# Kernel tuning notes

Measured on AMD Instinct MI355X. Metric: run time of the kernel, lower is better.

Reference implementation:

```python
import jax, jax.numpy as jnp
import numpy as np

B, S, D, H = 128, 256, 256, 8   # graphs, nodes/graph, dim_h, heads
N = B * S
E = 524288
DH = D // H
BN_EPS = 1e-5

def _bn(v, g, b):
    # BatchNorm1d forward with batch statistics (biased var), eval-dropout model
    m = v.mean(0)
    var = v.var(0)
    return (v - m) * jax.lax.rsqrt(var + BN_EPS) * g + b

def setup_inputs() -> dict:
    key = jax.random.key(0)
    ks = jax.random.split(key, 40)
    x = jax.random.normal(ks[0], (N, D), jnp.float32)
    src = jax.random.randint(ks[1], (E,), 0, N)
    dst = (src // S) * S + jax.random.randint(ks[2], (E,), 0, S)  # intra-graph edges
    edge_index = jnp.stack([src, dst]).astype(jnp.int64)
    def lin(k, i, o):
        return (jax.random.normal(k, (i, o), jnp.float32) / np.float32(np.sqrt(i)))
    inp = {
        'x': x, 'edge_index': edge_index,
        'W_gcn': lin(ks[3], D, D), 'b_gcn': jnp.zeros((D,), jnp.float32),
        'W_gin1': lin(ks[4], D, D), 'b_gin1': jnp.zeros((D,), jnp.float32),
        'W_gin2': lin(ks[5], D, D), 'b_gin2': jnp.zeros((D,), jnp.float32),
        'g_kv': jnp.ones((D,), jnp.float32), 'be_kv': jnp.zeros((D,), jnp.float32),
        'Wq1': lin(ks[6], D, D), 'bq1': jnp.zeros((D,), jnp.float32),
        'Wq2': lin(ks[7], D, D), 'bq2': jnp.zeros((D,), jnp.float32),
        'Wq_a': lin(ks[8], D, D), 'bq_a': jnp.zeros((D,), jnp.float32),
        'Wk_a': lin(ks[9], D, D), 'bk_a': jnp.zeros((D,), jnp.float32),
        'Wv_a': lin(ks[10], D, D), 'bv_a': jnp.zeros((D,), jnp.float32),
        'Wo_a': lin(ks[11], D, D), 'bo_a': jnp.zeros((D,), jnp.float32),
        'g_attn': jnp.ones((D,), jnp.float32), 'be_attn': jnp.zeros((D,), jnp.float32),
        'Wf1': lin(ks[12], D, 2 * D), 'bf1': jnp.zeros((2 * D,), jnp.float32),
        'Wf2': lin(ks[13], 2 * D, D), 'bf2': jnp.zeros((D,), jnp.float32),
        'g2': jnp.ones((D,), jnp.float32), 'be2': jnp.zeros((D,), jnp.float32),
    }
    return inp

def _forward(x, edge_index,
             W_gcn, b_gcn, W_gin1, b_gin1, W_gin2, b_gin2, g_kv, be_kv,
             Wq1, bq1, Wq2, bq2,
             Wq_a, bq_a, Wk_a, bk_a, Wv_a, bv_a, Wo_a, bo_a, g_attn, be_attn,
             Wf1, bf1, Wf2, bf2, g2, be2):
    row, col = edge_index[0], edge_index[1]
    h_in1 = x

    # ---- expert 0: GCNConv (add self loops + symmetric norm) ----
    loops = jnp.arange(N, dtype=row.dtype)
    row2 = jnp.concatenate([row, loops])
    col2 = jnp.concatenate([col, loops])
    deg = jax.ops.segment_sum(jnp.ones_like(row2, jnp.float32), col2, num_segments=N)
    dinv = jnp.where(deg > 0, jax.lax.rsqrt(deg), 0.0)
    norm = dinv[row2] * dinv[col2]                     # [E+N]
    xw = x @ W_gcn                                      # [N, D]
    h_gcn = jax.ops.segment_sum(norm[:, None] * xw[row2], col2, num_segments=N) + b_gcn
    e0 = _bn(h_gcn, g_kv, be_kv)

    # ---- expert 1: GINConv (eps=0, sum aggregation, 2-layer MLP) ----
    agg = jax.ops.segment_sum(x[row], col, num_segments=N)
    h_gin = jax.nn.relu((x + agg) @ W_gin1 + b_gin1) @ W_gin2 + b_gin2
    e1 = _bn(h_gin, g_kv, be_kv)

    # ---- global expert normalization (torch .std -> unbiased) ----
    allo = jnp.concatenate([e0, e1], axis=0)
    gm = allo.mean()
    gs = jnp.std(allo, ddof=1)
    e0 = (e0 - gm) / (gs + 1e-8)
    e1 = (e1 - gm) / (gs + 1e-8)

    # ---- uniform routing & kv residual mix ----
    kv = 0.5 * e0 + 0.5 * e1 + 0.1 * h_in1              # [N, D]

    # ---- dense batching (equal-sized graphs -> pure reshape, full mask) ----
    q_dense = h_in1.reshape(B, S, D)
    kv_dense = kv.reshape(B, S, D)

    # ---- q projection MLP ----
    q_dense = jax.nn.relu(q_dense @ Wq1 + bq1) @ Wq2 + bq2

    # ---- multihead attention (batch_first, no padding) ----
    qh = (q_dense @ Wq_a + bq_a).reshape(B, S, H, DH)
    kh = (kv_dense @ Wk_a + bk_a).reshape(B, S, H, DH)
    vh = (kv_dense @ Wv_a + bv_a).reshape(B, S, H, DH)
    scores = jnp.einsum('bqhd,bkhd->bhqk', qh, kh) / np.float32(np.sqrt(DH))
    attn = jax.nn.softmax(scores, axis=-1)
    o = jnp.einsum('bhqk,bkhd->bqhd', attn, vh).reshape(B, S, D)
    h_attn = (o @ Wo_a + bo_a).reshape(N, D)

    # ---- residual + norm + FFN block ----
    h = _bn(h_in1 + h_attn, g_attn, be_attn)
    h_ff = jax.nn.relu(h @ Wf1 + bf1) @ Wf2 + bf2
    h = _bn(h + h_ff, g2, be2)
    return h

def reference(x, edge_index,
              W_gcn, b_gcn, W_gin1, b_gin1, W_gin2, b_gin2, g_kv, be_kv,
              Wq1, bq1, Wq2, bq2,
              Wq_a, bq_a, Wk_a, bk_a, Wv_a, bv_a, Wo_a, bo_a, g_attn, be_attn,
              Wf1, bf1, Wf2, bf2, g2, be2):
    return _forward(x, edge_index,
                    W_gcn, b_gcn, W_gin1, b_gin1, W_gin2, b_gin2, g_kv, be_kv,
                    Wq1, bq1, Wq2, bq2,
                    Wq_a, bq_a, Wk_a, bk_a, Wv_a, bv_a, Wo_a, bo_a, g_attn, be_attn,
                    Wf1, bf1, Wf2, bf2, g2, be2)
```

## Files before the change

kernel.cpp:

```cpp
#include <hip/hip_runtime.h>
#include <hip/hip_bf16.h>

typedef __hip_bfloat16 bf16;
typedef __attribute__((ext_vector_type(8))) short short8;
typedef __attribute__((ext_vector_type(4))) short short4v;
typedef __attribute__((ext_vector_type(4))) float f32x4;

#define N_ 32768
#define D_ 256
#define S_ 256
#define B_ 128
#define E_ 524288

static __device__ __forceinline__ f32x4 mfma16(short8 a, short8 b, f32x4 c) {
  return __builtin_amdgcn_mfma_f32_16x16x32_bf16(a, b, c, 0, 0, 0);
}
static __device__ __forceinline__ f32x4 fzero4() {
  f32x4 z; z[0] = 0.f; z[1] = 0.f; z[2] = 0.f; z[3] = 0.f; return z;
}
static __device__ __forceinline__ float bits2f(short s) {
  unsigned u = ((unsigned)(unsigned short)s) << 16;
  return __builtin_bit_cast(float, u);
}
static __device__ __forceinline__ short f2bits(float f) {
  bf16 b = __float2bfloat16(f);
  return __builtin_bit_cast(short, b);
}
static __device__ __forceinline__ float tof(float x) { return x; }
static __device__ __forceinline__ float tof(bf16 x) { return __bfloat162float(x); }

#define GLOAD_LDS16(G, L) __builtin_amdgcn_global_load_lds( \
    (const __attribute__((address_space(1))) void*)(G),     \
    (__attribute__((address_space(3))) void*)(L), 16, 0, 0)

template<int F>
__global__ __launch_bounds__(256)
void gemm_bt(const bf16* __restrict__ A, const bf16* __restrict__ Bt,
             const float* __restrict__ bias, const void* __restrict__ resid,
             float* __restrict__ Cf, bf16* __restrict__ Cb,
             float* __restrict__ Sp, float* __restrict__ SSp,
             int M, int Nc, int K, long bsA, long bsB, long bsC)
{
  __shared__ __align__(16) bf16 lA[128 * 32];
  __shared__ __align__(16) bf16 lB[128 * 32];
  __shared__ float sS[2][128], sSS[2][128];
  const int z = blockIdx.z;
  const bf16* Ab = A + (long)z * bsA;
  const bf16* Bb = Bt + (long)z * bsB;
  const int m0 = blockIdx.x * 128, n0 = blockIdx.y * 128;
  const int tid = threadIdx.x;
  const int lane = tid & 63;
  const int w = tid >> 6, wr = w >> 1, wc = w & 1;
  const int g = lane >> 4, r = lane & 15, ko = g * 8;
  const int srow = lane >> 2, skw = (lane & 3) * 8;

  f32x4 acc[4][4];
  for (int i = 0; i < 4; i++) for (int j = 0; j < 4; j++) acc[i][j] = fzero4();

  for (int k0 = 0; k0 < K; k0 += 32) {
    __syncthreads();
    for (int i = 0; i < 2; i++) {
      const int c = w * 2 + i;
      GLOAD_LDS16(Ab + (long)(m0 + c * 16 + srow) * K + k0 + skw, lA + c * 512);
      GLOAD_LDS16(Bb + (long)(n0 + c * 16 + srow) * K + k0 + skw, lB + c * 512);
    }
    __syncthreads();
    short8 af[4], bfv[4];
    for (int mi = 0; mi < 4; mi++)
      af[mi] = *(const short8*)&lA[(wr * 64 + mi * 16 + r) * 32 + ko];
    for (int ni = 0; ni < 4; ni++)
      bfv[ni] = *(const short8*)&lB[(wc * 64 + ni * 16 + r) * 32 + ko];
    for (int mi = 0; mi < 4; mi++)
      for (int ni = 0; ni < 4; ni++)
        acc[mi][ni] = mfma16(af[mi], bfv[ni], acc[mi][ni]);
  }

  float cs[4] = {0, 0, 0, 0}, css[4] = {0, 0, 0, 0};
  for (int mi = 0; mi < 4; mi++) for (int ni = 0; ni < 4; ni++) {
    const int row = m0 + wr * 64 + mi * 16 + g * 4;
    const int col = n0 + wc * 64 + ni * 16 + r;
    float bv = (F & 2) ? bias[col] : 0.0f;
    for (int j = 0; j < 4; j++) {
      long idx = (long)(row + j) * Nc + col;
      float v = acc[mi][ni][j] + bv;
      if (F & 4)  v += ((const float*)resid)[(long)z * bsC + idx];
      if (F & 64) v += bits2f(((const short*)resid)[(long)z * bsC + idx]);
      if (F & 1)  v = fmaxf(v, 0.0f);
      if (F & 32) { cs[ni] += v; css[ni] += v * v; }
      if (F & 8)  Cf[(long)z * bsC + idx] = v;
      if (F & 16) Cb[(long)z * bsC + idx] = __float2bfloat16(v);
    }
  }
  if (F & 32) {
    for (int ni = 0; ni < 4; ni++) {
      cs[ni]  += __shfl_xor(cs[ni], 16);  cs[ni]  += __shfl_xor(cs[ni], 32);
      css[ni] += __shfl_xor(css[ni], 16); css[ni] += __shfl_xor(css[ni], 32);
    }
    if (lane < 16) {
      for (int ni = 0; ni < 4; ni++) {
        sS[wr][wc * 64 + ni * 16 + lane]  = cs[ni];
        sSS[wr][wc * 64 + ni * 16 + lane] = css[ni];
      }
    }
    __syncthreads();
    if (tid < 128) {
      atomicAdd(&Sp[n0 + tid],  sS[0][tid] + sS[1][tid]);
      atomicAdd(&SSp[n0 + tid], sSS[0][tid] + sSS[1][tid]);
    }
  }
}

__global__ __launch_bounds__(256)
void attn_k(const bf16* __restrict__ qh, const bf16* __restrict__ kh,
            const bf16* __restrict__ vh, bf16* __restrict__ ob)
{
  const int qt = blockIdx.x, h = blockIdx.y, b = blockIdx.z;
  const int tid = threadIdx.x, lane = tid & 63, w = tid >> 6;
  const int g = lane >> 4, r = lane & 15, ko = g * 8;
  __shared__ __align__(16) bf16 lQ[64 * 40];
  __shared__ __align__(16) bf16 lK[256 * 40];
  __shared__ __align__(16) bf16 lV[32 * 264];
  __shared__ __align__(16) bf16 lP[4][16 * 264];

  { int row = tid >> 2, c = (tid & 3) * 8;
    *(short8*)&lQ[row * 40 + c] =
      *(const short8*)(qh + (long)(b * 256 + qt * 64 + row) * 256 + h * 32 + c); }
  for (int i = 0; i < 4; i++) {
    int s = tid + i * 256; int row = s >> 2, c = (s & 3) * 8;
    *(short8*)&lK[row * 40 + c] =
      *(const short8*)(kh + (long)(b * 256 + row) * 256 + h * 32 + c);
  }
  const bf16* vbp = vh + (long)b * 65536 + h * 32;
  for (int i = 0; i < 4; i++) {
    int q = tid + i * 256;
    int s = q >> 2, part = q & 3;
    short8 v = *(const short8*)(vbp + (long)s * 256 + part * 8);
    for (int j = 0; j < 8; j++)
      ((short*)lV)[(part * 8 + j) * 264 + s] = v[j];
  }
  __syncthreads();

  short8 aq = *(const short8*)&lQ[(w * 16 + r) * 40 + ko];
  f32x4 sc[16];
  for (int nc = 0; nc < 16; nc++) {
    short8 bk = *(const short8*)&lK[(nc * 16 + r) * 40 + ko];
    sc[nc] = mfma16(aq, bk, fzero4());
  }
  const float scale = 0.17677669529663687f;
  float rsum[4];
  for (int j = 0; j < 4; j++) {
    float mx = -3.4e38f;
    for (int nc = 0; nc < 16; nc++) mx = fmaxf(mx, sc[nc][j]);
    mx = fmaxf(mx, __shfl_xor(mx, 1));
    mx = fmaxf(mx, __shfl_xor(mx, 2));
    mx = fmaxf(mx, __shfl_xor(mx, 4));
    mx = fmaxf(mx, __shfl_xor(mx, 8));
    float sum = 0.f;
    for (int nc = 0; nc < 16; nc++) {
      float p = __expf((sc[nc][j] - mx) * scale);
      sc[nc][j] = p; sum += p;
    }
    sum += __shfl_xor(sum, 1); sum += __shfl_xor(sum, 2);
    sum += __shfl_xor(sum, 4); sum += __shfl_xor(sum, 8);
    rsum[j] = sum;
    for (int nc = 0; nc < 16; nc++)
      lP[w][(g * 4 + j) * 264 + nc * 16 + r] = __float2bfloat16(sc[nc][j]);
  }
  __syncthreads();
  f32x4 oa[2]; oa[0] = fzero4(); oa[1] = fzero4();
  for (int kc = 0; kc < 8; kc++) {
    short8 ap = *(const short8*)&lP[w][r * 264 + kc * 32 + ko];
    for (int n = 0; n < 2; n++) {
      short8 bv = *(const short8*)&lV[(n * 16 + r) * 264 + kc * 32 + ko];
      oa[n] = mfma16(ap, bv, oa[n]);
    }
  }
  for (int n = 0; n < 2; n++) for (int j = 0; j < 4; j++) {
    float v = oa[n][j] / rsum[j];
    ob[(long)(b * 256 + qt * 64 + w * 16 + g * 4 + j) * 256 + h * 32 + n * 16 + r] =
      __float2bfloat16(v);
  }
}

template<typename TIN>
__global__ __launch_bounds__(256)
void transpose_cast_k(const TIN* __restrict__ in, bf16* __restrict__ out,
                      int in_rs, int out_rs, long zhi, long out_zs)
{
  __shared__ float tile[32][33];
  const int z = blockIdx.z;
  const long ioff = (long)z * zhi;
  const long ooff = (long)z * out_zs;
  const int tx = threadIdx.x, ty = threadIdx.y;
  const int c = blockIdx.x * 32 + tx;
  const int rb = blockIdx.y * 32;
  for (int i = 0; i < 4; i++)
    tile[ty + i * 8][tx] = tof(in[ioff + (long)(rb + ty + i * 8) * in_rs + c]);
  __syncthreads();
  const int oc = rb + tx;
  const int orb = blockIdx.x * 32;
  for (int i = 0; i < 4; i++)
    out[ooff + (long)(orb + ty + i * 8) * out_rs + oc] =
      __float2bfloat16(tile[tx][ty + i * 8]);
}

__global__ __launch_bounds__(256)
void w9t_k(const float* w0, const float* w1, const float* w2, const float* w3,
           const float* w4, const float* w5, const float* w6, const float* w7,
           const float* w8, bf16* __restrict__ out)
{
  __shared__ float tile[32][33];
  const float* srcs[9] = {w0, w1, w2, w3, w4, w5, w6, w7, w8};
  const int wi = blockIdx.z;
  const float* in = srcs[wi];
  bf16* o = out + (long)wi * 65536;
  const int tx = threadIdx.x, ty = threadIdx.y;
  const int c = blockIdx.x * 32 + tx;
  const int rb = blockIdx.y * 32;
  for (int i = 0; i < 4; i++)
    tile[ty + i * 8][tx] = in[(rb + ty + i * 8) * 256 + c];
  __syncthreads();
  const int oc = rb + tx;
  const int orb = blockIdx.x * 32;
  for (int i = 0; i < 4; i++)
    o[(orb + ty + i * 8) * 256 + oc] = __float2bfloat16(tile[tx][ty + i * 8]);
}

__global__ __launch_bounds__(256)
void cast4_k(const float* __restrict__ in, bf16* __restrict__ out)
{
  long i = ((long)blockIdx.x * 256 + threadIdx.x) * 4;
  float4 v = *(const float4*)(in + i);
  short4v o;
  o[0] = f2bits(v.x); o[1] = f2bits(v.y); o[2] = f2bits(v.z); o[3] = f2bits(v.w);
  *(short4v*)(out + i) = o;
}

__global__ __launch_bounds__(256)
void edge_cnt_k(const int* __restrict__ ei, float* __restrict__ cnt)
{
  int e = blockIdx.x * 256 + threadIdx.x;
  int src = ei[e], dst = ei[E_ + e];
  long idx = ((long)(src >> 8) * 256 + (dst & 255)) * 256 + (src & 255);
  atomicAdd(&cnt[idx], 1.0f);
}

__global__ __launch_bounds__(256)
void deg_k(const float* __restrict__ cnt, float* __restrict__ dinv)
{
  int rid = blockIdx.x * 16 + (threadIdx.x >> 4);
  int l16 = threadIdx.x & 15;
  const float4* rp = (const float4*)(cnt + (long)rid * 256);
  float s = 0.f;
  for (int i = 0; i < 4; i++) {
    float4 v = rp[l16 + i * 16];
    s += v.x + v.y + v.z + v.w;
  }
  s += __shfl_xor(s, 1); s += __shfl_xor(s, 2);
  s += __shfl_xor(s, 4); s += __shfl_xor(s, 8);
  if (l16 == 0) dinv[rid] = rsqrtf(s + 1.0f);
}

__global__ __launch_bounds__(256)
void adj_derive_k(const float* __restrict__ cnt, const float* __restrict__ dinv,
                  bf16* __restrict__ gin, bf16* __restrict__ gcn)
{
  long i = ((long)blockIdx.x * 256 + threadIdx.x) * 4;
  float4 c = *(const float4*)(cnt + i);
  long row = i >> 8;
  int g = (int)(row >> 8), dst = (int)(row & 255);
  int src0 = (int)(i & 255);
  float dd = dinv[row];
  const float* ds = dinv + (long)g * 256 + src0;
  float cv[4] = {c.x, c.y, c.z, c.w};
  short4v oi, oc;
  for (int j = 0; j < 4; j++) {
    float gv = cv[j] * dd * ds[j];
    if (src0 + j == dst) gv += dd * dd;
    oi[j] = f2bits(cv[j]);
    oc[j] = f2bits(gv);
  }
  *(short4v*)(gin + i) = oi;
  *(short4v*)(gcn + i) = oc;
}

__global__ __launch_bounds__(256)
void expert_stats_k(const float* __restrict__ S0, const float* __restrict__ SS0,
                    const float* __restrict__ S1, const float* __restrict__ SS1,
                    const float* __restrict__ gkv, const float* __restrict__ bkv,
                    float* __restrict__ kA, float* __restrict__ kB,
                    float* __restrict__ kC)
{
  const int d = threadIdx.x;
  const float invN = 1.0f / 32768.0f;
  float m0 = S0[d] * invN, v0 = SS0[d] * invN - m0 * m0;
  float a0 = gkv[d] * rsqrtf(v0 + 1e-5f), c0 = bkv[d] - m0 * a0;
  float m1 = S1[d] * invN, v1 = SS1[d] * invN - m1 * m1;
  float a1 = gkv[d] * rsqrtf(v1 + 1e-5f), c1 = bkv[d] - m1 * a1;
  float gsum = a0 * S0[d] + 32768.0f * c0 + a1 * S1[d] + 32768.0f * c1;
  float gss  = a0 * a0 * SS0[d] + 2.0f * a0 * c0 * S0[d] + 32768.0f * c0 * c0
             + a1 * a1 * SS1[d] + 2.0f * a1 * c1 * S1[d] + 32768.0f * c1 * c1;
  __shared__ float r1[256], r2[256];
  r1[d] = gsum; r2[d] = gss;
  __syncthreads();
  for (int s = 128; s > 0; s >>= 1) {
    if (d < s) { r1[d] += r1[d + s]; r2[d] += r2[d + s]; }
    __syncthreads();
  }
  const float cntall = 16777216.0f;
  float tg = r1[0], tss = r2[0];
  float gm = tg / cntall;
  float var = (tss - tg * tg / cntall) / (cntall - 1.0f);
  float gs = sqrtf(fmaxf(var, 0.f)) + 1e-8f;
  kA[d] = 0.5f * a0 / gs;
  kB[d] = 0.5f * a1 / gs;
  kC[d] = 0.5f * (c0 + c1 - 2.0f * gm) / gs;
}

__global__ __launch_bounds__(256)
void kv_mix_k(const bf16* __restrict__ hgcn, const bf16* __restrict__ hgin,
              const bf16* __restrict__ xb, const float* __restrict__ kA,
              const float* __restrict__ kB, const float* __restrict__ kC,
              bf16* __restrict__ kv)
{
  long i = ((long)blockIdx.x * 256 + threadIdx.x) * 8;
  int d0 = (int)(i & 255);
  short8 a = *(const short8*)(hgcn + i);
  short8 b = *(const short8*)(hgin + i);
  short8 c = *(const short8*)(xb + i);
  short8 o;
  for (int j = 0; j < 8; j++) {
    int d = d0 + j;
    float v = kA[d] * bits2f(a[j]) + kB[d] * bits2f(b[j]) + kC[d] + 0.1f * bits2f(c[j]);
    o[j] = f2bits(v);
  }
  *(short8*)(kv + i) = o;
}

template<int MODE>
__global__ __launch_bounds__(256)
void bn_apply_k(const bf16* __restrict__ in, const float* __restrict__ S,
                const float* __restrict__ SSq, const float* __restrict__ gg,
                const float* __restrict__ bb, float* __restrict__ outf,
                bf16* __restrict__ outb)
{
  long i = ((long)blockIdx.x * 256 + threadIdx.x) * 8;
  int d0 = (int)(i & 255);
  short8 v = *(const short8*)(in + i);
  const float invN = 1.0f / 32768.0f;
  float4 o0, o1; short8 o8;
  for (int j = 0; j < 8; j++) {
    int d = d0 + j;
    float m = S[d] * invN;
    float var = SSq[d] * invN - m * m;
    float a = gg[d] * rsqrtf(var + 1e-5f);
    float c = bb[d] - m * a;
    float o = a * bits2f(v[j]) + c;
    if (MODE & 1) { if (j < 4) (&o0.x)[j] = o; else (&o1.x)[j - 4] = o; }
    if (MODE & 2) o8[j] = f2bits(o);
  }
  if (MODE & 1) { *(float4*)(outf + i) = o0; *(float4*)(outf + i + 4) = o1; }
  if (MODE & 2) *(short8*)(outb + i) = o8;
}

static constexpr size_t OFF_S0 = 0, OFF_SS0 = 1024, OFF_S1 = 2048, OFF_SS1 = 3072;
static constexpr size_t OFF_S2 = 4096, OFF_SS2 = 5120, OFF_S3 = 6144, OFF_SS3 = 7168;
static constexpr size_t OFF_KA = 8192, OFF_KB = 9216, OFF_KC = 10240;
static constexpr size_t OFF_CNT = 16384;
static constexpr size_t ADJ_BYTES = (size_t)B_ * S_ * S_ * 4;
static constexpr size_t ZERO_BYTES = OFF_CNT + ADJ_BYTES;
static constexpr size_t OFF_DINV = ZERO_BYTES;
static constexpr size_t OFF_W = OFF_DINV + 131072;
static constexpr size_t NDB2 = (size_t)N_ * D_ * 2;
static constexpr size_t OFF_ADJGINB = OFF_W + 1703936;
static constexpr size_t OFF_ADJGCNB = OFF_ADJGINB + NDB2;
static constexpr size_t OFF_XB   = OFF_ADJGCNB + NDB2;
static constexpr size_t OFF_XT   = OFF_XB + NDB2;
static constexpr size_t OFF_XWB  = OFF_XT + NDB2;
static constexpr size_t OFF_XWT  = OFF_XWB + NDB2;
static constexpr size_t OFF_KV   = OFF_XWT + NDB2;
static constexpr size_t OFF_HGCN = OFF_KV + NDB2;
static constexpr size_t OFF_HGIN = OFF_HGCN + NDB2;

extern "C" void kernel_launch(void* const* d_in, const int* in_sizes, int n_in,
                              void* d_out, int out_size, void* d_ws, size_t ws_size,
                              hipStream_t stream)
{
  (void)in_sizes; (void)n_in; (void)out_size; (void)ws_size;
  const float* x      = (const float*)d_in[0];
  const int*   ei     = (const int*)d_in[1];
  const float* W_gcn  = (const float*)d_in[2];
  const float* b_gcn  = (const float*)d_in[3];
  const float* W_gin1 = (const float*)d_in[4];
  const float* b_gin1 = (const float*)d_in[5];
  const float* W_gin2 = (const float*)d_in[6];
  const float* b_gin2 = (const float*)d_in[7];
  const float* g_kv   = (const float*)d_in[8];
  const float* be_kv  = (const float*)d_in[9];
  const float* Wq1    = (const float*)d_in[10];
  const float* bq1    = (const float*)d_in[11];
  const float* Wq2    = (const float*)d_in[12];
  const float* bq2    = (const float*)d_in[13];
  const float* Wq_a   = (const float*)d_in[14];
  const float* bq_a   = (const float*)d_in[15];
  const float* Wk_a   = (const float*)d_in[16];
  const float* bk_a   = (const float*)d_in[17];
  const float* Wv_a   = (const float*)d_in[18];
  const float* bv_a   = (const float*)d_in[19];
  const float* Wo_a   = (const float*)d_in[20];
  const float* bo_a   = (const float*)d_in[21];
  const float* g_attn = (const float*)d_in[22];
  const float* be_attn= (const float*)d_in[23];
  const float* Wf1    = (const float*)d_in[24];
  const float* bf1    = (const float*)d_in[25];
  const float* Wf2    = (const float*)d_in[26];
  const float* bf2    = (const float*)d_in[27];
  const float* g2     = (const float*)d_in[28];
  const float* be2    = (const float*)d_in[29];

  char* ws = (char*)d_ws;
  float* S0  = (float*)(ws + OFF_S0);  float* SS0 = (float*)(ws + OFF_SS0);
  float* S1  = (float*)(ws + OFF_S1);  float* SS1 = (float*)(ws + OFF_SS1);
  float* S2  = (float*)(ws + OFF_S2);  float* SS2 = (float*)(ws + OFF_SS2);
  float* S3  = (float*)(ws + OFF_S3);  float* SS3 = (float*)(ws + OFF_SS3);
  float* kA  = (float*)(ws + OFF_KA);  float* kB  = (float*)(ws + OFF_KB);
  float* kC  = (float*)(ws + OFF_KC);
  float* cntA = (float*)(ws + OFF_CNT);
  float* dinv = (float*)(ws + OFF_DINV);
  bf16* wT = (bf16*)(ws + OFF_W);
  bf16 *WgcnT = wT,            *Wgin1T = wT + 65536,  *Wgin2T = wT + 131072;
  bf16 *Wq1T  = wT + 196608,   *Wq2T   = wT + 262144, *WqaT   = wT + 327680;
  bf16 *WkaT  = wT + 393216,   *WvaT   = wT + 458752, *WoaT   = wT + 524288;
  bf16 *Wf1T  = wT + 589824,   *Wf2T   = wT + 720896;
  bf16* adjGINb = (bf16*)(ws + OFF_ADJGINB);
  bf16* adjGCNb = (bf16*)(ws + OFF_ADJGCNB);
  bf16* xb    = (bf16*)(ws + OFF_XB);
  bf16* xT    = (bf16*)(ws + OFF_XT);
  bf16* xw_bf = (bf16*)(ws + OFF_XWB);
  bf16* xwT   = (bf16*)(ws + OFF_XWT);
  bf16* kv_bf = (bf16*)(ws + OFF_KV);
  bf16* hgcnb = (bf16*)(ws + OFF_HGCN);
  bf16* hginb = (bf16*)(ws + OFF_HGIN);
  bf16* gin_in = xw_bf;
  bf16* gin_h  = adjGCNb;
  bf16* qhb    = adjGCNb;
  bf16* khb    = adjGINb;
  bf16* q1b    = xT;
  bf16* qb     = xw_bf;
  bf16* vhb    = hgcnb;
  bf16* ob     = hginb;
  bf16* tbufb  = (bf16*)(ws + OFF_CNT);
  bf16* hb     = xb;
  bf16* f1b    = (bf16*)(ws + OFF_XWT);
  bf16* t2b    = adjGCNb;
  float* outp  = (float*)d_out;

  hipMemsetAsync(d_ws, 0, ZERO_BYTES, stream);

  dim3 tb(32, 8);
  w9t_k<<<dim3(8, 8, 9), tb, 0, stream>>>(W_gcn, W_gin1, W_gin2, Wq1, Wq2,
                                          Wq_a, Wk_a, Wv_a, Wo_a, wT);
  transpose_cast_k<float><<<dim3(16, 8, 1), tb, 0, stream>>>(Wf1, Wf1T, 512, 256, 0, 0);
  transpose_cast_k<float><<<dim3(8, 16, 1), tb, 0, stream>>>(Wf2, Wf2T, 256, 512, 0, 0);
  cast4_k<<<8192, 256, 0, stream>>>(x, xb);
  transpose_cast_k<float><<<dim3(8, 8, 128), tb, 0, stream>>>(x, xT, 256, 256, 65536, 65536);
  edge_cnt_k<<<2048, 256, 0, stream>>>(ei, cntA);
  deg_k<<<2048, 256, 0, stream>>>(cntA, dinv);
  adj_derive_k<<<8192, 256, 0, stream>>>(cntA, dinv, adjGINb, adjGCNb);
  gemm_bt<16><<<dim3(256, 2, 1), 256, 0, stream>>>(xb, WgcnT, nullptr, nullptr,
      nullptr, xw_bf, nullptr, nullptr, N_, 256, 256, 0, 0, 0);
  transpose_cast_k<bf16><<<dim3(8, 8, 128), tb, 0, stream>>>(xw_bf, xwT, 256, 256, 65536, 65536);
  gemm_bt<50><<<dim3(2, 2, 128), 256, 0, stream>>>(adjGCNb, xwT, b_gcn, nullptr,
      nullptr, hgcnb, S0, SS0, 256, 256, 256, 65536, 65536, 65536);
  gemm_bt<80><<<dim3(2, 2, 128), 256, 0, stream>>>(adjGINb, xT, nullptr, xb,
      nullptr, gin_in, nullptr, nullptr, 256, 256, 256, 65536, 65536, 65536);
  gemm_bt<19><<<dim3(256, 2, 1), 256, 0, stream>>>(gin_in, Wgin1T, b_gin1, nullptr,
      nullptr, gin_h, nullptr, nullptr, N_, 256, 256, 0, 0, 0);
  gemm_bt<50><<<dim3(256, 2, 1), 256, 0, stream>>>(gin_h, Wgin2T, b_gin2, nullptr,
      nullptr, hginb, S1, SS1, N_, 256, 256, 0, 0, 0);
  expert_stats_k<<<1, 256, 0, stream>>>(S0, SS0, S1, SS1, g_kv, be_kv, kA, kB, kC);
  kv_mix_k<<<4096, 256, 0, stream>>>(hgcnb, hginb, xb, kA, kB, kC, kv_bf);
  gemm_bt<19><<<dim3(256, 2, 1), 256, 0, stream>>>(xb, Wq1T, bq1, nullptr,
      nullptr, q1b, nullptr, nullptr, N_, 256, 256, 0, 0, 0);
  gemm_bt<18><<<dim3(256, 2, 1), 256, 0, stream>>>(q1b, Wq2T, bq2, nullptr,
      nullptr, qb, nullptr, nullptr, N_, 256, 256, 0, 0, 0);
  gemm_bt<18><<<dim3(256, 2, 1), 256, 0, stream>>>(qb, WqaT, bq_a, nullptr,
      nullptr, qhb, nullptr, nullptr, N_, 256, 256, 0, 0, 0);
  gemm_bt<18><<<dim3(256, 2, 1), 256, 0, stream>>>(kv_bf, WkaT, bk_a, nullptr,
      nullptr, khb, nullptr, nullptr, N_, 256, 256, 0, 0, 0);
  gemm_bt<18><<<dim3(256, 2, 1), 256, 0, stream>>>(kv_bf, WvaT, bv_a, nullptr,
      nullptr, vhb, nullptr, nullptr, N_, 256, 256, 0, 0, 0);
  attn_k<<<dim3(4, 8, 128), 256, 0, stream>>>(qhb, khb, vhb, ob);
  gemm_bt<114><<<dim3(256, 2, 1), 256, 0, stream>>>(ob, WoaT, bo_a, xb,
      nullptr, tbufb, S2, SS2, N_, 256, 256, 0, 0, 0);
  bn_apply_k<2><<<4096, 256, 0, stream>>>(tbufb, S2, SS2, g_attn, be_attn, nullptr, hb);
  gemm_bt<19><<<dim3(256, 4, 1), 256, 0, stream>>>(hb, Wf1T, bf1, nullptr,
      nullptr, f1b, nullptr, nullptr, N_, 512, 256, 0, 0, 0);
  gemm_bt<114><<<dim3(256, 2, 1), 256, 0, stream>>>(f1b, Wf2T, bf2, hb,
      nullptr, t2b, S3, SS3, N_, 256, 512, 0, 0, 0);
  bn_apply_k<1><<<4096, 256, 0, stream>>>(t2b, S3, SS3, g2, be2, outp, nullptr);
}
```

Before: 377.7 us.

## Process all query rows per attention block and pack edge counts as 16-bit

The attention kernel now launches one block per (head, graph) instead of four query tiles, so K and V are staged into shared memory once and each wave loops over four 16-row query chunks, loading Q straight from global. This removes the redundant K/V loads and the transposed V scatter that each query tile used to repeat, but the grid shrinks to 1024 blocks and each block does serial work. Separately, edge counts are stored as two packed 16-bit integers per 32-bit word, which halves the zero-fill and the cnt traffic in deg/adj_derive. Packed counts overflow if any (dst, src) pair receives 65536 or more edges.

```diff
diff --git a/kernel.cpp b/kernel.cpp
--- a/kernel.cpp
+++ b/kernel.cpp
@@ -114,17 +114,13 @@
 void attn_k(const bf16* __restrict__ qh, const bf16* __restrict__ kh,
             const bf16* __restrict__ vh, bf16* __restrict__ ob)
 {
-  const int qt = blockIdx.x, h = blockIdx.y, b = blockIdx.z;
+  const int h = blockIdx.x, b = blockIdx.y;
   const int tid = threadIdx.x, lane = tid & 63, w = tid >> 6;
   const int g = lane >> 4, r = lane & 15, ko = g * 8;
-  __shared__ __align__(16) bf16 lQ[64 * 40];
   __shared__ __align__(16) bf16 lK[256 * 40];
   __shared__ __align__(16) bf16 lV[32 * 264];
   __shared__ __align__(16) bf16 lP[4][16 * 264];
 
-  { int row = tid >> 2, c = (tid & 3) * 8;
-    *(short8*)&lQ[row * 40 + c] =
-      *(const short8*)(qh + (long)(b * 256 + qt * 64 + row) * 256 + h * 32 + c); }
   for (int i = 0; i < 4; i++) {
     int s = tid + i * 256; int row = s >> 2, c = (s & 3) * 8;
     *(short8*)&lK[row * 40 + c] =
@@ -140,45 +136,46 @@
   }
   __syncthreads();
 
-  short8 aq = *(const short8*)&lQ[(w * 16 + r) * 40 + ko];
-  f32x4 sc[16];
-  for (int nc = 0; nc < 16; nc++) {
-    short8 bk = *(const short8*)&lK[(nc * 16 + r) * 40 + ko];
-    sc[nc] = mfma16(aq, bk, fzero4());
-  }
   const float scale = 0.17677669529663687f;
-  float rsum[4];
-  for (int j = 0; j < 4; j++) {
-    float mx = -3.4e38f;
-    for (int nc = 0; nc < 16; nc++) mx = fmaxf(mx, sc[nc][j]);
-    mx = fmaxf(mx, __shfl_xor(mx, 1));
-    mx = fmaxf(mx, __shfl_xor(mx, 2));
-    mx = fmaxf(mx, __shfl_xor(mx, 4));
-    mx = fmaxf(mx, __shfl_xor(mx, 8));
-    float sum = 0.f;
+  for (int mc = 0; mc < 4; mc++) {
+    const long qrow = (long)b * 256 + w * 64 + mc * 16;
+    short8 aq = *(const short8*)(qh + (qrow + r) * 256 + h * 32 + ko);
+    f32x4 sc[16];
     for (int nc = 0; nc < 16; nc++) {
-      float p = __expf((sc[nc][j] - mx) * scale);
-      sc[nc][j] = p; sum += p;
-    }
-    sum += __shfl_xor(sum, 1); sum += __shfl_xor(sum, 2);
-    sum += __shfl_xor(sum, 4); sum += __shfl_xor(sum, 8);
-    rsum[j] = sum;
-    for (int nc = 0; nc < 16; nc++)
-      lP[w][(g * 4 + j) * 264 + nc * 16 + r] = __float2bfloat16(sc[nc][j]);
-  }
-  __syncthreads();
-  f32x4 oa[2]; oa[0] = fzero4(); oa[1] = fzero4();
-  for (int kc = 0; kc < 8; kc++) {
-    short8 ap = *(const short8*)&lP[w][r * 264 + kc * 32 + ko];
-    for (int n = 0; n < 2; n++) {
-      short8 bv = *(const short8*)&lV[(n * 16 + r) * 264 + kc * 32 + ko];
-      oa[n] = mfma16(ap, bv, oa[n]);
-    }
-  }
-  for (int n = 0; n < 2; n++) for (int j = 0; j < 4; j++) {
-    float v = oa[n][j] / rsum[j];
-    ob[(long)(b * 256 + qt * 64 + w * 16 + g * 4 + j) * 256 + h * 32 + n * 16 + r] =
-      __float2bfloat16(v);
+      short8 bk = *(const short8*)&lK[(nc * 16 + r) * 40 + ko];
+      sc[nc] = mfma16(aq, bk, fzero4());
+    }
+    float rsum[4];
+    for (int j = 0; j < 4; j++) {
+      float mx = -3.4e38f;
+      for (int nc = 0; nc < 16; nc++) mx = fmaxf(mx, sc[nc][j]);
+      mx = fmaxf(mx, __shfl_xor(mx, 1));
+      mx = fmaxf(mx, __shfl_xor(mx, 2));
+      mx = fmaxf(mx, __shfl_xor(mx, 4));
+      mx = fmaxf(mx, __shfl_xor(mx, 8));
+      float sum = 0.f;
+      for (int nc = 0; nc < 16; nc++) {
+        float p = __expf((sc[nc][j] - mx) * scale);
+        sc[nc][j] = p; sum += p;
+      }
+      sum += __shfl_xor(sum, 1); sum += __shfl_xor(sum, 2);
+      sum += __shfl_xor(sum, 4); sum += __shfl_xor(sum, 8);
+      rsum[j] = sum;
+      for (int nc = 0; nc < 16; nc++)
+        lP[w][(g * 4 + j) * 264 + nc * 16 + r] = __float2bfloat16(sc[nc][j]);
+    }
+    f32x4 oa[2]; oa[0] = fzero4(); oa[1] = fzero4();
+    for (int kc = 0; kc < 8; kc++) {
+      short8 ap = *(const short8*)&lP[w][r * 264 + kc * 32 + ko];
+      for (int n = 0; n < 2; n++) {
+        short8 bv = *(const short8*)&lV[(n * 16 + r) * 264 + kc * 32 + ko];
+        oa[n] = mfma16(ap, bv, oa[n]);
+      }
+    }
+    for (int n = 0; n < 2; n++) for (int j = 0; j < 4; j++) {
+      float v = oa[n][j] / rsum[j];
+      ob[(qrow + g * 4 + j) * 256 + h * 32 + n * 16 + r] = __float2bfloat16(v);
+    }
   }
 }
 
@@ -237,42 +234,44 @@
 }
 
 __global__ __launch_bounds__(256)
-void edge_cnt_k(const int* __restrict__ ei, float* __restrict__ cnt)
+void edge_cnt_k(const int* __restrict__ ei, unsigned* __restrict__ cnt)
 {
   int e = blockIdx.x * 256 + threadIdx.x;
   int src = ei[e], dst = ei[E_ + e];
   long idx = ((long)(src >> 8) * 256 + (dst & 255)) * 256 + (src & 255);
-  atomicAdd(&cnt[idx], 1.0f);
-}
-
-__global__ __launch_bounds__(256)
-void deg_k(const float* __restrict__ cnt, float* __restrict__ dinv)
+  atomicAdd(&cnt[idx >> 1], 1u << ((idx & 1) * 16));
+}
+
+__global__ __launch_bounds__(256)
+void deg_k(const unsigned* __restrict__ cnt, float* __restrict__ dinv)
 {
   int rid = blockIdx.x * 16 + (threadIdx.x >> 4);
   int l16 = threadIdx.x & 15;
-  const float4* rp = (const float4*)(cnt + (long)rid * 256);
-  float s = 0.f;
-  for (int i = 0; i < 4; i++) {
-    float4 v = rp[l16 + i * 16];
-    s += v.x + v.y + v.z + v.w;
+  const uint4* rp = (const uint4*)(cnt + (long)rid * 128);
+  unsigned s = 0;
+  for (int i = 0; i < 2; i++) {
+    uint4 v = rp[l16 + i * 16];
+    s += (v.x & 0xFFFF) + (v.x >> 16) + (v.y & 0xFFFF) + (v.y >> 16)
+       + (v.z & 0xFFFF) + (v.z >> 16) + (v.w & 0xFFFF) + (v.w >> 16);
   }
   s += __shfl_xor(s, 1); s += __shfl_xor(s, 2);
   s += __shfl_xor(s, 4); s += __shfl_xor(s, 8);
-  if (l16 == 0) dinv[rid] = rsqrtf(s + 1.0f);
-}
-
-__global__ __launch_bounds__(256)
-void adj_derive_k(const float* __restrict__ cnt, const float* __restrict__ dinv,
+  if (l16 == 0) dinv[rid] = rsqrtf((float)s + 1.0f);
+}
+
+__global__ __launch_bounds__(256)
+void adj_derive_k(const unsigned* __restrict__ cnt, const float* __restrict__ dinv,
                   bf16* __restrict__ gin, bf16* __restrict__ gcn)
 {
   long i = ((long)blockIdx.x * 256 + threadIdx.x) * 4;
-  float4 c = *(const float4*)(cnt + i);
+  uint2 cp = *(const uint2*)(cnt + (i >> 1));
+  float cv[4] = {(float)(cp.x & 0xFFFF), (float)(cp.x >> 16),
+                 (float)(cp.y & 0xFFFF), (float)(cp.y >> 16)};
   long row = i >> 8;
   int g = (int)(row >> 8), dst = (int)(row & 255);
   int src0 = (int)(i & 255);
   float dd = dinv[row];
   const float* ds = dinv + (long)g * 256 + src0;
-  float cv[4] = {c.x, c.y, c.z, c.w};
   short4v oi, oc;
   for (int j = 0; j < 4; j++) {
     float gv = cv[j] * dd * ds[j];
@@ -367,8 +366,8 @@
 static constexpr size_t OFF_S2 = 4096, OFF_SS2 = 5120, OFF_S3 = 6144, OFF_SS3 = 7168;
 static constexpr size_t OFF_KA = 8192, OFF_KB = 9216, OFF_KC = 10240;
 static constexpr size_t OFF_CNT = 16384;
-static constexpr size_t ADJ_BYTES = (size_t)B_ * S_ * S_ * 4;
-static constexpr size_t ZERO_BYTES = OFF_CNT + ADJ_BYTES;
+static constexpr size_t CNT_BYTES = (size_t)B_ * S_ * S_ * 2;
+static constexpr size_t ZERO_BYTES = OFF_CNT + CNT_BYTES;
 static constexpr size_t OFF_DINV = ZERO_BYTES;
 static constexpr size_t OFF_W = OFF_DINV + 131072;
 static constexpr size_t NDB2 = (size_t)N_ * D_ * 2;
@@ -425,7 +424,7 @@
   float* S3  = (float*)(ws + OFF_S3);  float* SS3 = (float*)(ws + OFF_SS3);
   float* kA  = (float*)(ws + OFF_KA);  float* kB  = (float*)(ws + OFF_KB);
   float* kC  = (float*)(ws + OFF_KC);
-  float* cntA = (float*)(ws + OFF_CNT);
+  unsigned* cntA = (unsigned*)(ws + OFF_CNT);
   float* dinv = (float*)(ws + OFF_DINV);
   bf16* wT = (bf16*)(ws + OFF_W);
   bf16 *WgcnT = wT,            *Wgin1T = wT + 65536,  *Wgin2T = wT + 131072;
@@ -490,7 +489,7 @@
       nullptr, khb, nullptr, nullptr, N_, 256, 256, 0, 0, 0);
   gemm_bt<18><<<dim3(256, 2, 1), 256, 0, stream>>>(kv_bf, WvaT, bv_a, nullptr,
       nullptr, vhb, nullptr, nullptr, N_, 256, 256, 0, 0, 0);
-  attn_k<<<dim3(4, 8, 128), 256, 0, stream>>>(qhb, khb, vhb, ob);
+  attn_k<<<dim3(8, 128), 256, 0, stream>>>(qhb, khb, vhb, ob);
   gemm_bt<114><<<dim3(256, 2, 1), 256, 0, stream>>>(ob, WoaT, bo_a, xb,
       nullptr, tbufb, S2, SS2, N_, 256, 256, 0, 0, 0);
   bn_apply_k<2><<<4096, 256, 0, stream>>>(tbufb, S2, SS2, g_attn, be_attn, nullptr, hb);
```

New measurement: 354.5 us. 1.07x faster.
